# Performance work log

Hardware: AMD Instinct MI355X
Metric: run time of the kernel (lower is better)

## Reference

```python
import jax, jax.numpy as jnp
import numpy as np

IN_F = 4096
OUT_F = 4096
GS = 128  # group size for int4 scales


def setup_inputs() -> dict:
    key = jax.random.key(0)
    ks = jax.random.split(key, 5)
    x = jax.random.normal(ks[0], (4, 2048, IN_F), dtype=jnp.float32)
    # each byte packs two unsigned int4 values (low nibble = even col, high nibble = odd col)
    w_packed = jax.random.randint(ks[1], (OUT_F, IN_F // 2), 0, 256, dtype=jnp.int32)
    w_scales = jax.random.uniform(ks[2], (OUT_F, IN_F // GS), dtype=jnp.float32,
                                  minval=0.005, maxval=0.02)
    perm = jax.random.permutation(ks[3], IN_F).astype(jnp.int32)
    bias = jax.random.normal(ks[4], (OUT_F,), dtype=jnp.float32) * 0.01
    return {"x": x, "w_packed": w_packed, "w_scales": w_scales, "perm": perm, "bias": bias}


def _dequantize_groupwise_int4(w_packed, w_scales):
    # unpack two int4 values per byte, zero-point 8 -> symmetric range [-8, 7]
    low = (w_packed & 0xF) - 8
    high = ((w_packed >> 4) & 0xF) - 8
    q = jnp.stack([low, high], axis=-1).reshape(OUT_F, IN_F).astype(jnp.float32)
    # apply one scale per group of GS input features
    w = q.reshape(OUT_F, IN_F // GS, GS) * w_scales[:, :, None]
    return w.reshape(OUT_F, IN_F)  # [out_features, in_features]


def reference(x, w_packed, w_scales, perm, bias):
    shape = x.shape
    xf = x.reshape(-1, IN_F)[:, perm]          # activation permutation (GPTQ act-order)
    w = _dequantize_groupwise_int4(w_packed, w_scales)
    y = xf @ w.T                               # [tokens, out_features]
    return y.reshape(*shape[:-1], OUT_F) + bias
```

## Files before the change

### kernel.cpp

```cpp
#include <hip/hip_runtime.h>

#define IN_F 4096
#define OUT_F 4096
#define GS 128

#define BM 256
#define BN 256
#define BKB 128
#define NT (IN_F / BKB)
#define BUFB (BM * BKB)

typedef int i32x4 __attribute__((ext_vector_type(4)));

typedef __attribute__((address_space(1))) void void_g;
typedef __attribute__((address_space(3))) void void_l;

__device__ __forceinline__ void async_copy16(void* lds, const void* g) {
  __builtin_amdgcn_global_load_lds((const void_g*)g, (void_l*)lds, 16, 0, 0);
}

__device__ __forceinline__ void stage_g(signed char* region, int rowbase,
                                        const signed char* mat, int k0,
                                        int wave, int growl, int gcolb) {
  async_copy16(region + rowbase * BKB + wave * 1024,
               mat + (size_t)(rowbase + growl) * IN_F + k0 + gcolb);
}

__global__ void invperm_kernel(const int* __restrict__ perm, int* __restrict__ inv) {
  int i = blockIdx.x * blockDim.x + threadIdx.x;
  inv[perm[i]] = i;
}

__global__ __launch_bounds__(256) void prep_kernel(
    const float* __restrict__ x,
    unsigned int* __restrict__ xq4,
    float* __restrict__ sx,
    const int* __restrict__ wp,
    const float* __restrict__ wsc,
    const int* __restrict__ inv,
    unsigned int* __restrict__ wq4,
    float* __restrict__ sw,
    int M)
{
  __shared__ unsigned int prow[IN_F / 2];
  __shared__ float srow[IN_F / GS];
  __shared__ float red[256];
  const int tid = threadIdx.x;
  const int b = blockIdx.x;

  if (b < M) {
    const float4* x4 = (const float4*)(x + (size_t)b * IN_F);
    float4 v[4];
    float m = 0.f;
#pragma unroll
    for (int i = 0; i < 4; ++i) {
      v[i] = x4[tid + i * 256];
      m = fmaxf(m, fmaxf(fmaxf(fabsf(v[i].x), fabsf(v[i].y)),
                         fmaxf(fabsf(v[i].z), fabsf(v[i].w))));
    }
    red[tid] = m;
    __syncthreads();
#pragma unroll
    for (int s = 128; s > 0; s >>= 1) {
      if (tid < s) red[tid] = fmaxf(red[tid], red[tid + s]);
      __syncthreads();
    }
    const float mx = red[0];
    const float r = 127.0f / mx;
    if (tid == 0) sx[b] = mx * (1.0f / 127.0f);

    unsigned int* orow = xq4 + (size_t)b * (IN_F / 4);
#pragma unroll
    for (int i = 0; i < 4; ++i) {
      int q0 = (int)rintf(v[i].x * r);
      int q1 = (int)rintf(v[i].y * r);
      int q2 = (int)rintf(v[i].z * r);
      int q3 = (int)rintf(v[i].w * r);
      orow[tid + i * 256] = (unsigned)(q0 & 0xFF) | ((unsigned)(q1 & 0xFF) << 8) |
                            ((unsigned)(q2 & 0xFF) << 16) | ((unsigned)(q3 & 0xFF) << 24);
    }
  } else {
    const int o = b - M;
    const int4* wp4 = (const int4*)(wp + (size_t)o * (IN_F / 2));
    int4* p4 = (int4*)prow;
#pragma unroll
    for (int i = 0; i < 2; ++i)
      p4[tid + i * 256] = wp4[tid + i * 256];
    if (tid < IN_F / GS) srow[tid] = wsc[o * (IN_F / GS) + tid];
    __syncthreads();

    float m = 0.f;
#pragma unroll
    for (int c = 0; c < 8; ++c) {
      const int p = tid + c * 256;
      const unsigned bb = prow[p];
      const float s = srow[p >> 6];
      const float lo = (float)((int)(bb & 0xFu) - 8);
      const float hi = (float)((int)((bb >> 4) & 0xFu) - 8);
      m = fmaxf(m, fmaxf(fabsf(lo), fabsf(hi)) * s);
    }
    red[tid] = m;
    __syncthreads();
#pragma unroll
    for (int s = 128; s > 0; s >>= 1) {
      if (tid < s) red[tid] = fmaxf(red[tid], red[tid + s]);
      __syncthreads();
    }
    const float wmax = red[0];
    const float r = (wmax > 0.f) ? 127.0f / wmax : 0.f;
    if (tid == 0) sw[o] = wmax * (1.0f / 127.0f);

    unsigned int* orow = wq4 + (size_t)o * (IN_F / 4);
    const int4* inv4 = (const int4*)inv;
#pragma unroll
    for (int c = 0; c < 4; ++c) {
      const int p = tid + c * 256;
      const int4 iv = inv4[p];
      unsigned out = 0;
      const int idx[4] = {iv.x, iv.y, iv.z, iv.w};
#pragma unroll
      for (int e = 0; e < 4; ++e) {
        const int ii = idx[e];
        const unsigned wbits = prow[ii >> 1];
        const int n = (int)((wbits >> ((ii & 1) * 4)) & 0xFu) - 8;
        const float v = (float)n * srow[ii >> 7] * r;
        const int q = (int)rintf(v);
        out |= (unsigned)(q & 0xFF) << (e * 8);
      }
      orow[p] = out;
    }
  }
}

template <bool LAST>
__device__ __forceinline__ void gemm_tile(
    const signed char* Ac, const signed char* Bc,
    signed char* An, signed char* Bn,
    const signed char* a_base, const signed char* b_base, int k0n,
    int wave, int wm, int wn, int l16, int quad, int sxz,
    int growl, int gcolb, i32x4 (&acc)[8][4])
{
  i32x4 bq[4][2];
#pragma unroll
  for (int p = 0; p < 4; ++p) {
    if (p == 0) {
#pragma unroll
      for (int j = 0; j < 4; ++j)
#pragma unroll
        for (int ks = 0; ks < 2; ++ks) {
          const int off = (wn + j * 16 + l16) * BKB + ((ks * 64 + quad * 16) ^ sxz);
          bq[j][ks] = *(const i32x4*)(Bc + off);
        }
    }
    i32x4 aq[2][2];
#pragma unroll
    for (int i = 0; i < 2; ++i)
#pragma unroll
      for (int ks = 0; ks < 2; ++ks) {
        const int off = (wm + p * 32 + i * 16 + l16) * BKB + ((ks * 64 + quad * 16) ^ sxz);
        aq[i][ks] = *(const i32x4*)(Ac + off);
      }
    if (!LAST) {
      if (p == 0) {
        stage_g(Bn, 0, b_base, k0n, wave, growl, gcolb);
        stage_g(Bn, 64, b_base, k0n, wave, growl, gcolb);
      } else if (p == 1) {
        stage_g(Bn, 128, b_base, k0n, wave, growl, gcolb);
        stage_g(Bn, 192, b_base, k0n, wave, growl, gcolb);
      } else if (p == 2) {
        stage_g(An, 0, a_base, k0n, wave, growl, gcolb);
        stage_g(An, 128, a_base, k0n, wave, growl, gcolb);
      } else {
        stage_g(An, 64, a_base, k0n, wave, growl, gcolb);
        stage_g(An, 192, a_base, k0n, wave, growl, gcolb);
      }
    }
    asm volatile("s_waitcnt lgkmcnt(0)" ::: "memory");
    __builtin_amdgcn_sched_barrier(0);
    __builtin_amdgcn_s_setprio(1);
#pragma unroll
    for (int i = 0; i < 2; ++i)
#pragma unroll
      for (int j = 0; j < 4; ++j)
#pragma unroll
        for (int ks = 0; ks < 2; ++ks)
          acc[2 * p + i][j] = __builtin_amdgcn_mfma_i32_16x16x64_i8(
              aq[i][ks], bq[j][ks], acc[2 * p + i][j], 0, 0, 0);
    __builtin_amdgcn_s_setprio(0);
    if (p == 1) {
      if (LAST) { asm volatile("s_waitcnt vmcnt(0)" ::: "memory"); }
      else      { asm volatile("s_waitcnt vmcnt(4)" ::: "memory"); }
      __builtin_amdgcn_sched_barrier(0);
      __builtin_amdgcn_s_barrier();
    } else if (p == 3) {
      if (!LAST) { asm volatile("s_waitcnt vmcnt(2)" ::: "memory"); }
      __builtin_amdgcn_sched_barrier(0);
      __builtin_amdgcn_s_barrier();
    }
  }
}

__global__ __launch_bounds__(512, 2) void gemm_kernel(
    const signed char* __restrict__ A,
    const signed char* __restrict__ B,
    const float* __restrict__ sx,
    const float* __restrict__ sw,
    const float* __restrict__ bias,
    float* __restrict__ C) {
  __shared__ signed char As[2 * BUFB];
  __shared__ signed char Bs[2 * BUFB];

  const int tid  = threadIdx.x;
  const int wave = tid >> 6;
  const int lane = tid & 63;
  const int quad = lane >> 4;
  const int l16  = lane & 15;

  const int bm = blockIdx.y;
  const int bn = blockIdx.x;
  const signed char* a_base = A + (size_t)bm * BM * IN_F;
  const signed char* b_base = B + (size_t)bn * BN * IN_F;

  const int wm = (wave >> 2) * 128;
  const int wn = (wave & 3) * 64;
  const int sxz = (l16 & 7) << 4;

  const int growl = tid >> 3;
  const int gcolb = ((tid & 7) ^ ((tid >> 3) & 7)) << 4;

  i32x4 acc[8][4] = {};

  stage_g(Bs, 0, b_base, 0, wave, growl, gcolb);
  stage_g(Bs, 64, b_base, 0, wave, growl, gcolb);
  stage_g(Bs, 128, b_base, 0, wave, growl, gcolb);
  stage_g(Bs, 192, b_base, 0, wave, growl, gcolb);
  stage_g(As, 0, a_base, 0, wave, growl, gcolb);
  stage_g(As, 128, a_base, 0, wave, growl, gcolb);
  stage_g(As, 64, a_base, 0, wave, growl, gcolb);
  stage_g(As, 192, a_base, 0, wave, growl, gcolb);
  asm volatile("s_waitcnt vmcnt(2)" ::: "memory");
  __builtin_amdgcn_sched_barrier(0);
  __builtin_amdgcn_s_barrier();

#pragma unroll 1
  for (int t = 0; t < NT - 1; ++t) {
    const int cur = t & 1;
    const int nxt = cur ^ 1;
    gemm_tile<false>(As + cur * BUFB, Bs + cur * BUFB,
                     As + nxt * BUFB, Bs + nxt * BUFB,
                     a_base, b_base, (t + 1) * BKB,
                     wave, wm, wn, l16, quad, sxz, growl, gcolb, acc);
  }
  gemm_tile<true>(As + ((NT - 1) & 1) * BUFB, Bs + ((NT - 1) & 1) * BUFB,
                  nullptr, nullptr, a_base, b_base, 0,
                  wave, wm, wn, l16, quad, sxz, growl, gcolb, acc);

  float* sxs = (float*)As;
  float* sws = sxs + BM;
  float* bsh = sws + BN;
  if (tid < BM) {
    sxs[tid] = sx[bm * BM + tid];
  } else {
    const int c = tid - BM;
    sws[c] = sw[bn * BN + c];
    bsh[c] = bias[bn * BN + c];
  }
  __syncthreads();

  const int wm_g = bm * BM + wm;
  const int wn_g = bn * BN + wn;
#pragma unroll
  for (int j = 0; j < 4; ++j) {
    const int col_l = wn + j * 16 + l16;
    const float swv = sws[col_l];
    const float bv  = bsh[col_l];
    const int col = wn_g + j * 16 + l16;
#pragma unroll
    for (int i = 0; i < 8; ++i) {
      const int row_l0 = wm + i * 16 + quad * 4;
      const int row0 = wm_g + i * 16 + quad * 4;
#pragma unroll
      for (int r = 0; r < 4; ++r)
        C[(size_t)(row0 + r) * OUT_F + col] =
            (float)acc[i][j][r] * (sxs[row_l0 + r] * swv) + bv;
    }
  }
}

extern "C" void kernel_launch(void* const* d_in, const int* in_sizes, int n_in,
                              void* d_out, int out_size, void* d_ws, size_t ws_size,
                              hipStream_t stream) {
  const float* x    = (const float*)d_in[0];
  const int*   wp   = (const int*)d_in[1];
  const float* wsc  = (const float*)d_in[2];
  const int*   perm = (const int*)d_in[3];
  const float* bias = (const float*)d_in[4];
  float* out = (float*)d_out;

  const int M = in_sizes[0] / IN_F;

  signed char* xq = (signed char*)d_ws;
  signed char* wq = xq + (size_t)M * IN_F;
  float* sx = (float*)(wq + (size_t)OUT_F * IN_F);
  float* sw = sx + M;
  int* inv = (int*)(sw + OUT_F);

  invperm_kernel<<<IN_F / 256, 256, 0, stream>>>(perm, inv);

  prep_kernel<<<M + OUT_F, 256, 0, stream>>>(
      x, (unsigned int*)xq, sx, wp, wsc, inv, (unsigned int*)wq, sw, M);

  dim3 grid(OUT_F / BN, M / BM);
  gemm_kernel<<<grid, 512, 0, stream>>>(xq, wq, sx, sw, bias, out);
}
```

Baseline: 382.2 us.

## Double-buffer A fragments in registers and reorder async stage schedule

```diff
diff --git a/kernel.cpp b/kernel.cpp
--- a/kernel.cpp
+++ b/kernel.cpp
@@ -138,44 +138,55 @@
     signed char* An, signed char* Bn,
     const signed char* a_base, const signed char* b_base, int k0n,
     int wave, int wm, int wn, int l16, int quad, int sxz,
-    int growl, int gcolb, i32x4 (&acc)[8][4])
+    int growl, int gcolb, i32x4 (&aq)[2][2][2], i32x4 (&bq)[4][2],
+    i32x4 (&acc)[8][4])
 {
-  i32x4 bq[4][2];
 #pragma unroll
   for (int p = 0; p < 4; ++p) {
+    const int cb = p & 1;
+    const int nb = cb ^ 1;
     if (p == 0) {
 #pragma unroll
       for (int j = 0; j < 4; ++j)
 #pragma unroll
-        for (int ks = 0; ks < 2; ++ks) {
-          const int off = (wn + j * 16 + l16) * BKB + ((ks * 64 + quad * 16) ^ sxz);
-          bq[j][ks] = *(const i32x4*)(Bc + off);
-        }
-    }
-    i32x4 aq[2][2];
-#pragma unroll
-    for (int i = 0; i < 2; ++i)
-#pragma unroll
-      for (int ks = 0; ks < 2; ++ks) {
-        const int off = (wm + p * 32 + i * 16 + l16) * BKB + ((ks * 64 + quad * 16) ^ sxz);
-        aq[i][ks] = *(const i32x4*)(Ac + off);
-      }
+        for (int ks = 0; ks < 2; ++ks)
+          bq[j][ks] = *(const i32x4*)(Bc + (wn + j * 16 + l16) * BKB +
+                                      ((ks * 64 + quad * 16) ^ sxz));
+      __builtin_amdgcn_sched_barrier(0);
+    }
+    if (p < 3) {
+#pragma unroll
+      for (int i = 0; i < 2; ++i)
+#pragma unroll
+        for (int ks = 0; ks < 2; ++ks)
+          aq[nb][i][ks] = *(const i32x4*)(Ac + (wm + (p + 1) * 32 + i * 16 + l16) * BKB +
+                                          ((ks * 64 + quad * 16) ^ sxz));
+    } else if (!LAST) {
+#pragma unroll
+      for (int i = 0; i < 2; ++i)
+#pragma unroll
+        for (int ks = 0; ks < 2; ++ks)
+          aq[nb][i][ks] = *(const i32x4*)(An + (wm + i * 16 + l16) * BKB +
+                                          ((ks * 64 + quad * 16) ^ sxz));
+    }
+    __builtin_amdgcn_sched_barrier(0);
     if (!LAST) {
       if (p == 0) {
         stage_g(Bn, 0, b_base, k0n, wave, growl, gcolb);
         stage_g(Bn, 64, b_base, k0n, wave, growl, gcolb);
       } else if (p == 1) {
+        stage_g(An, 0, a_base, k0n, wave, growl, gcolb);
+        stage_g(An, 128, a_base, k0n, wave, growl, gcolb);
+      } else if (p == 2) {
         stage_g(Bn, 128, b_base, k0n, wave, growl, gcolb);
         stage_g(Bn, 192, b_base, k0n, wave, growl, gcolb);
-      } else if (p == 2) {
-        stage_g(An, 0, a_base, k0n, wave, growl, gcolb);
-        stage_g(An, 128, a_base, k0n, wave, growl, gcolb);
       } else {
         stage_g(An, 64, a_base, k0n, wave, growl, gcolb);
         stage_g(An, 192, a_base, k0n, wave, growl, gcolb);
       }
     }
-    asm volatile("s_waitcnt lgkmcnt(0)" ::: "memory");
+    if (p == 3 && LAST) { asm volatile("s_waitcnt lgkmcnt(0)" ::: "memory"); }
+    else                { asm volatile("s_waitcnt lgkmcnt(4)" ::: "memory"); }
     __builtin_amdgcn_sched_barrier(0);
     __builtin_amdgcn_s_setprio(1);
 #pragma unroll
@@ -185,11 +196,15 @@
 #pragma unroll
         for (int ks = 0; ks < 2; ++ks)
           acc[2 * p + i][j] = __builtin_amdgcn_mfma_i32_16x16x64_i8(
-              aq[i][ks], bq[j][ks], acc[2 * p + i][j], 0, 0, 0);
+              aq[cb][i][ks], bq[j][ks], acc[2 * p + i][j], 0, 0, 0);
     __builtin_amdgcn_s_setprio(0);
-    if (p == 1) {
+    if (p == 0) {
       if (LAST) { asm volatile("s_waitcnt vmcnt(0)" ::: "memory"); }
-      else      { asm volatile("s_waitcnt vmcnt(4)" ::: "memory"); }
+      else      { asm volatile("s_waitcnt vmcnt(2)" ::: "memory"); }
+      __builtin_amdgcn_sched_barrier(0);
+      __builtin_amdgcn_s_barrier();
+    } else if (p == 2 && !LAST) {
+      asm volatile("s_waitcnt vmcnt(2)" ::: "memory");
       __builtin_amdgcn_sched_barrier(0);
       __builtin_amdgcn_s_barrier();
     } else if (p == 3) {
@@ -207,8 +222,8 @@
     const float* __restrict__ sw,
     const float* __restrict__ bias,
     float* __restrict__ C) {
-  __shared__ signed char As[2 * BUFB];
-  __shared__ signed char Bs[2 * BUFB];
+  __shared__ __align__(16) signed char As[2 * BUFB];
+  __shared__ __align__(16) signed char Bs[2 * BUFB];
 
   const int tid  = threadIdx.x;
   const int wave = tid >> 6;
@@ -229,6 +244,8 @@
   const int gcolb = ((tid & 7) ^ ((tid >> 3) & 7)) << 4;
 
   i32x4 acc[8][4] = {};
+  i32x4 aq[2][2][2];
+  i32x4 bq[4][2];
 
   stage_g(Bs, 0, b_base, 0, wave, growl, gcolb);
   stage_g(Bs, 64, b_base, 0, wave, growl, gcolb);
@@ -242,6 +259,13 @@
   __builtin_amdgcn_sched_barrier(0);
   __builtin_amdgcn_s_barrier();
 
+#pragma unroll
+  for (int i = 0; i < 2; ++i)
+#pragma unroll
+    for (int ks = 0; ks < 2; ++ks)
+      aq[0][i][ks] = *(const i32x4*)(As + (wm + i * 16 + l16) * BKB +
+                                     ((ks * 64 + quad * 16) ^ sxz));
+
 #pragma unroll 1
   for (int t = 0; t < NT - 1; ++t) {
     const int cur = t & 1;
@@ -249,11 +273,11 @@
     gemm_tile<false>(As + cur * BUFB, Bs + cur * BUFB,
                      As + nxt * BUFB, Bs + nxt * BUFB,
                      a_base, b_base, (t + 1) * BKB,
-                     wave, wm, wn, l16, quad, sxz, growl, gcolb, acc);
+                     wave, wm, wn, l16, quad, sxz, growl, gcolb, aq, bq, acc);
   }
   gemm_tile<true>(As + ((NT - 1) & 1) * BUFB, Bs + ((NT - 1) & 1) * BUFB,
                   nullptr, nullptr, a_base, b_base, 0,
-                  wave, wm, wn, l16, quad, sxz, growl, gcolb, acc);
+                  wave, wm, wn, l16, quad, sxz, growl, gcolb, aq, bq, acc);
 
   float* sxs = (float*)As;
   float* sws = sxs + BM;
```

Result: no change. 377.4 us (-1.3%).
